# Performance work log

Measured on AMD Instinct MI355X. Metric: run time of the kernel, lower is better.

## Reference

```python
import jax, jax.numpy as jnp
import numpy as np

MARGIN = 0.4
ALPHA = 1.0
B, D = 512, 512
NUM_CLASSES = 32


def setup_inputs() -> dict:
    key = jax.random.key(0)
    k1, k2 = jax.random.split(key)
    embeddings = jax.random.normal(k1, (B, D), dtype=jnp.float32)
    labels = jax.random.randint(k2, (B,), 0, NUM_CLASSES, dtype=jnp.int32)
    return {"embeddings": embeddings, "labels": labels}


def reference(embeddings, labels):
    # L2-normalize rows (F.normalize, p=2, dim=1)
    eps = 1e-12
    norm = jnp.sqrt(jnp.sum(embeddings * embeddings, axis=1, keepdims=True))
    x = embeddings / jnp.maximum(norm, eps)

    # Pairwise Euclidean distances (torch.cdist, p=2)
    sq = jnp.sum(x * x, axis=1)  # (B,)
    d2 = sq[:, None] + sq[None, :] - 2.0 * (x @ x.T)
    dist = jnp.sqrt(jnp.maximum(d2, 0.0))  # (B, B)

    same = labels[:, None] == labels[None, :]
    pos_mask = same & ~jnp.eye(labels.shape[0], dtype=bool)  # (B, B)
    neg_mask = ~same  # (B, B)

    # counts[i, j] = #{k : neg(i,k) and dist[i,k] < dist[i,j] + margin}
    # 3D broadcast replaces the original nested Python loops.
    viol = neg_mask[:, None, :] & (dist[:, None, :] < dist[:, :, None] + MARGIN)
    counts = jnp.sum(viol.astype(jnp.float32), axis=-1)  # (B, B)

    # Contribute log(1 + counts) * alpha only for positive pairs with > 0 violations
    contrib = jnp.where(pos_mask & (counts > 0), jnp.log1p(counts) * ALPHA, 0.0)
    n = jnp.float32(labels.shape[0])
    return jnp.sum(contrib) / (n + 1e-8)
```

## Files before the change

kernel.cpp:

```cpp
#include <hip/hip_runtime.h>
#include <math.h>

#define BSZ 512
#define DSZ 512
#define MARGIN 0.4f
#define ALPHA 1.0f

typedef unsigned int u32;
typedef __attribute__((ext_vector_type(8))) short bf16x8;
typedef __attribute__((ext_vector_type(4))) float f32x4;

static __device__ __forceinline__ u32 pack_bf16x2(float a, float b) {
    u32 ua = __float_as_uint(a);
    ua = (ua + 0x7fffu + ((ua >> 16) & 1u)) >> 16;
    u32 ub = __float_as_uint(b);
    ub = (ub + 0x7fffu + ((ub >> 16) & 1u)) & 0xffff0000u;
    return ua | ub;
}

__global__ __launch_bounds__(512) void rll_prep(const float* __restrict__ emb,
                                                u32* __restrict__ enr) {
    const int w = threadIdx.x >> 6, l = threadIdx.x & 63;
    const int r = blockIdx.x * 8 + w;
    const float4* src = (const float4*)(emb + (size_t)r * DSZ);
    float4 v0 = src[l * 2];
    float4 v1 = src[l * 2 + 1];
    float ss = v0.x * v0.x + v0.y * v0.y + v0.z * v0.z + v0.w * v0.w
             + v1.x * v1.x + v1.y * v1.y + v1.z * v1.z + v1.w * v1.w;
    #pragma unroll
    for (int off = 32; off > 0; off >>= 1) ss += __shfl_xor(ss, off);
    const float inv = 1.0f / fmaxf(sqrtf(ss), 1e-12f);
    v0.x *= inv; v0.y *= inv; v0.z *= inv; v0.w *= inv;
    v1.x *= inv; v1.y *= inv; v1.z *= inv; v1.w *= inv;
    *(uint4*)&enr[(size_t)r * 256 + l * 4] =
        make_uint4(pack_bf16x2(v0.x, v0.y), pack_bf16x2(v0.z, v0.w),
                   pack_bf16x2(v1.x, v1.y), pack_bf16x2(v1.z, v1.w));
}

__global__ __launch_bounds__(256) void rll_dist(const u32* __restrict__ enr,
                                                float* __restrict__ dist) {
    const int tid = threadIdx.x;
    const int w = tid >> 6, l = tid & 63;
    const int wr = w >> 1, wc = w & 1;
    const int brow = blockIdx.y * 32, bcol = blockIdx.x * 32;
    const int fr = l & 15;
    const int fk = (l >> 4) * 4;

    const u32* arow = enr + (size_t)(brow + wr * 16 + fr) * 256 + fk;
    const u32* brow_ = enr + (size_t)(bcol + wc * 16 + fr) * 256 + fk;

    bf16x8 afrag[16];
    #pragma unroll
    for (int kc = 0; kc < 16; ++kc)
        afrag[kc] = *(const bf16x8*)(arow + kc * 16);

    f32x4 acc = {0.f, 0.f, 0.f, 0.f};
    #pragma unroll
    for (int kc = 0; kc < 16; ++kc) {
        const bf16x8 b = *(const bf16x8*)(brow_ + kc * 16);
        acc = __builtin_amdgcn_mfma_f32_16x16x32_bf16(afrag[kc], b, acc, 0, 0, 0);
    }

    const int col = bcol + wc * 16 + fr;
    const int rowbase = brow + wr * 16 + ((l >> 4) << 2);
    #pragma unroll
    for (int r = 0; r < 4; ++r)
        dist[(size_t)(rowbase + r) * BSZ + col] =
            sqrtf(fmaxf(2.0f - 2.0f * acc[r], 0.0f));
}

__global__ __launch_bounds__(256) void rll_count(const float* __restrict__ dist,
                                                 const int* __restrict__ labels,
                                                 float* __restrict__ partial) {
    __shared__ float dsh[BSZ];
    __shared__ int   lsh[BSZ];
    __shared__ int   pos[128];
    __shared__ int   npos;
    __shared__ float wsum[4];
    const int i = blockIdx.x;
    const int tid = threadIdx.x;
    if (tid == 0) npos = 0;
    if (tid < 128) {
        *(float4*)&dsh[tid * 4] = ((const float4*)(dist + (size_t)i * BSZ))[tid];
        *(int4*)&lsh[tid * 4]   = ((const int4*)labels)[tid];
    }
    __syncthreads();
    const int li = lsh[i];
    for (int j = tid; j < BSZ; j += 256) {
        if (j != i && lsh[j] == li) {
            const int idx = atomicAdd(&npos, 1);
            if (idx < 128) pos[idx] = j;
        }
    }
    if (tid < 4) wsum[tid] = 0.f;
    __syncthreads();
    const int wave = tid >> 6, lane = tid & 63;
    const int np = min(npos, 128);
    float acc = 0.f;
    for (int p = wave; p < np; p += 4) {
        const int j = pos[p];
        const float thr = dsh[j] + MARGIN;
        int cnt = 0;
        #pragma unroll
        for (int q = 0; q < 8; ++q) {
            const int k = lane + q * 64;
            cnt += (lsh[k] != li && dsh[k] < thr) ? 1 : 0;
        }
        #pragma unroll
        for (int off = 32; off > 0; off >>= 1) cnt += __shfl_down(cnt, off);
        if (lane == 0 && cnt > 0) acc += log1pf((float)cnt);
    }
    if (lane == 0) wsum[wave] = acc;
    __syncthreads();
    if (tid == 0)
        partial[i] = wsum[0] + wsum[1] + wsum[2] + wsum[3];
}

__global__ __launch_bounds__(64) void rll_reduce(const float* __restrict__ partial,
                                                 float* __restrict__ out) {
    const int lane = threadIdx.x;
    float s = 0.f;
    #pragma unroll
    for (int q = 0; q < BSZ / 64; ++q) s += partial[lane + q * 64];
    #pragma unroll
    for (int off = 32; off > 0; off >>= 1) s += __shfl_down(s, off);
    if (lane == 0) out[0] = s * (ALPHA / (512.0f + 1e-8f));
}

extern "C" void kernel_launch(void* const* d_in, const int* in_sizes, int n_in,
                              void* d_out, int out_size, void* d_ws, size_t ws_size,
                              hipStream_t stream) {
    const float* emb    = (const float*)d_in[0];
    const int*   labels = (const int*)d_in[1];
    float* out = (float*)d_out;

    u32*   enr     = (u32*)d_ws;
    float* dist    = (float*)(enr + (size_t)BSZ * 256);
    float* partial = dist + (size_t)BSZ * BSZ;

    rll_prep<<<64, 512, 0, stream>>>(emb, enr);
    rll_dist<<<dim3(16, 16), 256, 0, stream>>>(enr, dist);
    rll_count<<<BSZ, 256, 0, stream>>>(dist, labels, partial);
    rll_reduce<<<1, 64, 0, stream>>>(partial, out);
}
```

Measured before the change: 25.73 us.

## Fuse normalization into distance kernel and final reduction into count kernel

Drops the separate prep kernel. The distance kernel now reads fp32 embeddings directly, packs them to bf16 in registers, and computes row norms alongside the MFMA loop, applying the inverse norms to the dot product afterwards. The final reduction kernel is also removed: the last count block, detected with an atomic counter, sums the partials. This cuts two kernel launches and the intermediate bf16 buffer. In exchange each tile re-reads fp32 rows (twice the bytes) and redoes the norm work, and normalization now happens after bf16 rounding rather than before, which slightly changes numerics.

Measured after the change: 32.57 us. +26.6%, slower.

```diff
diff --git a/kernel.cpp b/kernel.cpp
--- a/kernel.cpp
+++ b/kernel.cpp
@@ -18,65 +18,82 @@
     return ua | ub;
 }
 
-__global__ __launch_bounds__(512) void rll_prep(const float* __restrict__ emb,
-                                                u32* __restrict__ enr) {
-    const int w = threadIdx.x >> 6, l = threadIdx.x & 63;
-    const int r = blockIdx.x * 8 + w;
-    const float4* src = (const float4*)(emb + (size_t)r * DSZ);
-    float4 v0 = src[l * 2];
-    float4 v1 = src[l * 2 + 1];
-    float ss = v0.x * v0.x + v0.y * v0.y + v0.z * v0.z + v0.w * v0.w
-             + v1.x * v1.x + v1.y * v1.y + v1.z * v1.z + v1.w * v1.w;
-    #pragma unroll
-    for (int off = 32; off > 0; off >>= 1) ss += __shfl_xor(ss, off);
-    const float inv = 1.0f / fmaxf(sqrtf(ss), 1e-12f);
-    v0.x *= inv; v0.y *= inv; v0.z *= inv; v0.w *= inv;
-    v1.x *= inv; v1.y *= inv; v1.z *= inv; v1.w *= inv;
-    *(uint4*)&enr[(size_t)r * 256 + l * 4] =
-        make_uint4(pack_bf16x2(v0.x, v0.y), pack_bf16x2(v0.z, v0.w),
-                   pack_bf16x2(v1.x, v1.y), pack_bf16x2(v1.z, v1.w));
+static __device__ __forceinline__ bf16x8 pack8(const float4 a, const float4 b) {
+    union { u32 u[4]; bf16x8 v; } r;
+    r.u[0] = pack_bf16x2(a.x, a.y);
+    r.u[1] = pack_bf16x2(a.z, a.w);
+    r.u[2] = pack_bf16x2(b.x, b.y);
+    r.u[3] = pack_bf16x2(b.z, b.w);
+    return r.v;
 }
 
-__global__ __launch_bounds__(256) void rll_dist(const u32* __restrict__ enr,
-                                                float* __restrict__ dist) {
+__global__ __launch_bounds__(256) void rll_dist(const float* __restrict__ emb,
+                                                float* __restrict__ dist,
+                                                int* __restrict__ counter) {
+    __shared__ float invA[2][16];
+    __shared__ float invB[2][16];
     const int tid = threadIdx.x;
     const int w = tid >> 6, l = tid & 63;
     const int wr = w >> 1, wc = w & 1;
     const int brow = blockIdx.y * 32, bcol = blockIdx.x * 32;
     const int fr = l & 15;
-    const int fk = (l >> 4) * 4;
+    const int fkq = l >> 4;
+    if (blockIdx.x == 0 && blockIdx.y == 0 && tid == 0) counter[0] = 0;
 
-    const u32* arow = enr + (size_t)(brow + wr * 16 + fr) * 256 + fk;
-    const u32* brow_ = enr + (size_t)(bcol + wc * 16 + fr) * 256 + fk;
+    const float* arow = emb + (size_t)(brow + wr * 16 + fr) * DSZ + fkq * 8;
+    const float* brw  = emb + (size_t)(bcol + wc * 16 + fr) * DSZ + fkq * 8;
 
+    float ssa = 0.f, ssb = 0.f;
     bf16x8 afrag[16];
     #pragma unroll
-    for (int kc = 0; kc < 16; ++kc)
-        afrag[kc] = *(const bf16x8*)(arow + kc * 16);
-
+    for (int kc = 0; kc < 16; ++kc) {
+        const float4 a0 = *(const float4*)(arow + kc * 32);
+        const float4 a1 = *(const float4*)(arow + kc * 32 + 4);
+        ssa += a0.x * a0.x + a0.y * a0.y + a0.z * a0.z + a0.w * a0.w
+             + a1.x * a1.x + a1.y * a1.y + a1.z * a1.z + a1.w * a1.w;
+        afrag[kc] = pack8(a0, a1);
+    }
     f32x4 acc = {0.f, 0.f, 0.f, 0.f};
     #pragma unroll
     for (int kc = 0; kc < 16; ++kc) {
-        const bf16x8 b = *(const bf16x8*)(brow_ + kc * 16);
-        acc = __builtin_amdgcn_mfma_f32_16x16x32_bf16(afrag[kc], b, acc, 0, 0, 0);
+        const float4 b0 = *(const float4*)(brw + kc * 32);
+        const float4 b1 = *(const float4*)(brw + kc * 32 + 4);
+        ssb += b0.x * b0.x + b0.y * b0.y + b0.z * b0.z + b0.w * b0.w
+             + b1.x * b1.x + b1.y * b1.y + b1.z * b1.z + b1.w * b1.w;
+        acc = __builtin_amdgcn_mfma_f32_16x16x32_bf16(afrag[kc], pack8(b0, b1),
+                                                      acc, 0, 0, 0);
     }
 
+    ssa += __shfl_xor(ssa, 16); ssa += __shfl_xor(ssa, 32);
+    ssb += __shfl_xor(ssb, 16); ssb += __shfl_xor(ssb, 32);
+    if (l < 16) {
+        invA[wr][l] = 1.0f / fmaxf(sqrtf(ssa), 1e-12f);
+        invB[wc][l] = 1.0f / fmaxf(sqrtf(ssb), 1e-12f);
+    }
+    __syncthreads();
+
     const int col = bcol + wc * 16 + fr;
-    const int rowbase = brow + wr * 16 + ((l >> 4) << 2);
+    const int rloc = (l >> 4) << 2;
+    const int rowbase = brow + wr * 16 + rloc;
+    const float ib = invB[wc][fr];
     #pragma unroll
-    for (int r = 0; r < 4; ++r)
-        dist[(size_t)(rowbase + r) * BSZ + col] =
-            sqrtf(fmaxf(2.0f - 2.0f * acc[r], 0.0f));
+    for (int r = 0; r < 4; ++r) {
+        const float d = sqrtf(fmaxf(2.0f - 2.0f * acc[r] * invA[wr][rloc + r] * ib, 0.0f));
+        dist[(size_t)(rowbase + r) * BSZ + col] = d;
+    }
 }
 
 __global__ __launch_bounds__(256) void rll_count(const float* __restrict__ dist,
                                                  const int* __restrict__ labels,
-                                                 float* __restrict__ partial) {
+                                                 float* __restrict__ partial,
+                                                 int* __restrict__ counter,
+                                                 float* __restrict__ out) {
     __shared__ float dsh[BSZ];
     __shared__ int   lsh[BSZ];
     __shared__ int   pos[128];
     __shared__ int   npos;
     __shared__ float wsum[4];
+    __shared__ bool  last;
     const int i = blockIdx.x;
     const int tid = threadIdx.x;
     if (tid == 0) npos = 0;
@@ -112,19 +129,25 @@
     }
     if (lane == 0) wsum[wave] = acc;
     __syncthreads();
-    if (tid == 0)
+    if (tid == 0) {
         partial[i] = wsum[0] + wsum[1] + wsum[2] + wsum[3];
-}
-
-__global__ __launch_bounds__(64) void rll_reduce(const float* __restrict__ partial,
-                                                 float* __restrict__ out) {
-    const int lane = threadIdx.x;
-    float s = 0.f;
-    #pragma unroll
-    for (int q = 0; q < BSZ / 64; ++q) s += partial[lane + q * 64];
-    #pragma unroll
-    for (int off = 32; off > 0; off >>= 1) s += __shfl_down(s, off);
-    if (lane == 0) out[0] = s * (ALPHA / (512.0f + 1e-8f));
+        __threadfence();
+        const int old = atomicAdd(counter, 1);
+        last = (old == BSZ - 1);
+    }
+    __syncthreads();
+    if (last) {
+        __threadfence();
+        if (tid < 64) {
+            volatile const float* vp = (volatile const float*)partial;
+            float s = 0.f;
+            #pragma unroll
+            for (int q = 0; q < BSZ / 64; ++q) s += vp[tid + q * 64];
+            #pragma unroll
+            for (int off = 32; off > 0; off >>= 1) s += __shfl_down(s, off);
+            if (tid == 0) out[0] = s * (ALPHA / (512.0f + 1e-8f));
+        }
+    }
 }
 
 extern "C" void kernel_launch(void* const* d_in, const int* in_sizes, int n_in,
@@ -134,12 +157,10 @@
     const int*   labels = (const int*)d_in[1];
     float* out = (float*)d_out;
 
-    u32*   enr     = (u32*)d_ws;
-    float* dist    = (float*)(enr + (size_t)BSZ * 256);
+    float* dist    = (float*)d_ws;
     float* partial = dist + (size_t)BSZ * BSZ;
+    int*   counter = (int*)(partial + BSZ);
 
-    rll_prep<<<64, 512, 0, stream>>>(emb, enr);
-    rll_dist<<<dim3(16, 16), 256, 0, stream>>>(enr, dist);
-    rll_count<<<BSZ, 256, 0, stream>>>(dist, labels, partial);
-    rll_reduce<<<1, 64, 0, stream>>>(partial, out);
+    rll_dist<<<dim3(16, 16), 256, 0, stream>>>(emb, dist, counter);
+    rll_count<<<BSZ, 256, 0, stream>>>(dist, labels, partial, counter, out);
 }
```
